# Optimization experiments

Measured on AMD Instinct MI355X. Metric: run time of the kernel, lower is better.

## Reference

```python
import jax, jax.numpy as jnp
import numpy as np

B, S, D, H = 4, 2048, 1024, 16
HD = D // H
EPS = 1e-5

def _ln(x, g, b):
    mu = jnp.mean(x, axis=-1, keepdims=True)
    var = jnp.mean(jnp.square(x - mu), axis=-1, keepdims=True)
    return (x - mu) * jax.lax.rsqrt(var + EPS) * g + b

def setup_inputs() -> dict:
    key = jax.random.key(0)
    ks = jax.random.split(key, 6)
    W = 0.02  # GPT-2 style init scale keeps softmax unsaturated
    causal = jnp.tril(jnp.ones((S, S), dtype=bool))
    mask = jnp.where(causal, 0.0, -1e9).astype(jnp.float32)[None, None]
    return {
        "x": jax.random.normal(ks[0], (B, S, D), jnp.float32),
        "attention_mask": mask,
        "ln1_g": jnp.ones((D,), jnp.float32),
        "ln1_b": jnp.zeros((D,), jnp.float32),
        "w_qkv": jax.random.normal(ks[1], (D, 3 * D), jnp.float32) * W,
        "b_qkv": jnp.zeros((3 * D,), jnp.float32),
        "w_ao": jax.random.normal(ks[2], (D, D), jnp.float32) * W,
        "b_ao": jnp.zeros((D,), jnp.float32),
        "ln2_g": jnp.ones((D,), jnp.float32),
        "ln2_b": jnp.zeros((D,), jnp.float32),
        "w_fc": jax.random.normal(ks[3], (D, 4 * D), jnp.float32) * W,
        "b_fc": jnp.zeros((4 * D,), jnp.float32),
        "w_out": jax.random.normal(ks[4], (4 * D, D), jnp.float32) * W,
        "b_out": jnp.zeros((D,), jnp.float32),
    }

def reference(x, attention_mask, ln1_g, ln1_b, w_qkv, b_qkv, w_ao, b_ao,
              ln2_g, ln2_b, w_fc, b_fc, w_out, b_out):
    b, s, d = x.shape
    h = _ln(x, ln1_g, ln1_b)
    qkv = h @ w_qkv + b_qkv  # [B,S,3D]
    q, k, v = jnp.split(qkv, 3, axis=-1)
    def heads(t):  # [B,S,D] -> [B,H,S,HD]
        return t.reshape(b, s, H, HD).transpose(0, 2, 1, 3)
    q, k, v = heads(q), heads(k), heads(v)
    att = jnp.einsum('bhqd,bhkd->bhqk', q, k) / jnp.sqrt(jnp.float32(HD))
    att = att + attention_mask
    att = jax.nn.softmax(att, axis=-1)
    out = jnp.einsum('bhqk,bhkd->bhqd', att, v)
    out = out.transpose(0, 2, 1, 3).reshape(b, s, d)
    x = x + out @ w_ao + b_ao
    h2 = _ln(x, ln2_g, ln2_b)
    # torch nn.GELU() default is exact erf gelu
    mlp = jax.nn.gelu(h2 @ w_fc + b_fc, approximate=False) @ w_out + b_out
    return x + mlp
```

## Files before the change

kernel.cpp:

```cpp
#include <hip/hip_runtime.h>

typedef unsigned short u16;
typedef __attribute__((ext_vector_type(8))) short short8;
typedef __attribute__((ext_vector_type(4))) float floatx4;

#define S_LEN 2048
#define DMODEL 1024
#define NHEAD 16
#define HDIM 64

__device__ __forceinline__ u16 f2bf(float f) {
    union { float f; unsigned u; } v; v.f = f;
    unsigned u = v.u;
    unsigned r = (u + 0x7fffu + ((u >> 16) & 1u)) >> 16;
    return (u16)r;
}

__device__ __forceinline__ u16 f2bf_fast(float f) {
    union { float f; unsigned u; } v; v.f = f;
    return (u16)((v.u + 0x8000u) >> 16);
}

__device__ __forceinline__ void gld_lds16(const u16* g, u16* l) {
    __builtin_amdgcn_global_load_lds((const __attribute__((address_space(1))) void*)g,
                                     (__attribute__((address_space(3))) void*)l,
                                     16, 0, 0);
}

__global__ __launch_bounds__(256) void ln_kernel(
    const float* __restrict__ x, const float* __restrict__ g,
    const float* __restrict__ b, u16* __restrict__ out)
{
    int row = blockIdx.x;
    int tid = threadIdx.x;
    const float4* xr = (const float4*)(x + (size_t)row * DMODEL);
    float4 v = xr[tid];
    float s  = v.x + v.y + v.z + v.w;
    float s2 = v.x * v.x + v.y * v.y + v.z * v.z + v.w * v.w;
    #pragma unroll
    for (int off = 1; off < 64; off <<= 1) {
        s  += __shfl_xor(s, off, 64);
        s2 += __shfl_xor(s2, off, 64);
    }
    __shared__ float red[2][4];
    int w = tid >> 6, lane = tid & 63;
    if (lane == 0) { red[0][w] = s; red[1][w] = s2; }
    __syncthreads();
    s  = red[0][0] + red[0][1] + red[0][2] + red[0][3];
    s2 = red[1][0] + red[1][1] + red[1][2] + red[1][3];
    float mu  = s * (1.0f / DMODEL);
    float var = s2 * (1.0f / DMODEL) - mu * mu;
    float inv = rsqrtf(var + 1e-5f);
    const float4* gr = (const float4*)g;
    const float4* br = (const float4*)b;
    float4 gv = gr[tid], bv = br[tid];
    u16* o = out + (size_t)row * DMODEL + tid * 4;
    o[0] = f2bf((v.x - mu) * inv * gv.x + bv.x);
    o[1] = f2bf((v.y - mu) * inv * gv.y + bv.y);
    o[2] = f2bf((v.z - mu) * inv * gv.z + bv.z);
    o[3] = f2bf((v.w - mu) * inv * gv.w + bv.w);
}

__global__ __launch_bounds__(256) void transpose_cast(
    const float* __restrict__ w, u16* __restrict__ wt, int K, int N)
{
    __shared__ float t[32][33];
    int n0 = blockIdx.x * 32, k0 = blockIdx.y * 32;
    int x = threadIdx.x, y = threadIdx.y;
    #pragma unroll
    for (int j = y; j < 32; j += 8)
        t[j][x] = w[(size_t)(k0 + j) * N + n0 + x];
    __syncthreads();
    #pragma unroll
    for (int j = y; j < 32; j += 8)
        wt[(size_t)(n0 + j) * K + k0 + x] = f2bf(t[x][j]);
}

__global__ __launch_bounds__(256) void transpose_v(
    const u16* __restrict__ V, u16* __restrict__ Vt)
{
    __shared__ u16 t[64][66];
    int bh = blockIdx.y;
    int s0 = blockIdx.x * 64;
    int lane = threadIdx.x & 63, y = threadIdx.x >> 6;
    const u16* src = V + ((size_t)bh * S_LEN + s0) * HDIM;
    #pragma unroll
    for (int i = 0; i < 16; ++i) {
        int ss = y * 16 + i;
        t[ss][lane] = src[(size_t)ss * HDIM + lane];
    }
    __syncthreads();
    u16* dst = Vt + (size_t)bh * HDIM * S_LEN + s0;
    #pragma unroll
    for (int i = 0; i < 16; ++i) {
        int hd = y * 16 + i;
        dst[(size_t)hd * S_LEN + lane] = t[lane][hd];
    }
}

template<int MODE>
__global__ __launch_bounds__(256) void gemm_bt(
    const u16* __restrict__ A, const u16* __restrict__ BT,
    int M, int N, int K,
    const float* __restrict__ bias, const float* __restrict__ res,
    float* __restrict__ fout,
    u16* __restrict__ o0, u16* __restrict__ o1, u16* __restrict__ o2)
{
    __shared__ __attribute__((aligned(16))) u16 As[128 * 64];
    __shared__ __attribute__((aligned(16))) u16 Bs[128 * 64];
    int tid = threadIdx.x;
    int lane = tid & 63, w = tid >> 6;
    int wm = (w >> 1) * 64, wn = (w & 1) * 64;
    int l15 = lane & 15, quad = lane >> 4;
    int rowBase = blockIdx.y * 128, colBase = blockIdx.x * 128;

    floatx4 acc[4][4] = {};

    for (int k0 = 0; k0 < K; k0 += 64) {
        #pragma unroll
        for (int i = 0; i < 4; ++i) {
            int c  = i * 256 + tid;
            int cb = i * 256 + (tid & 0xC0);
            int r = c >> 3;
            int cs = (c & 7) ^ (r & 7);
            gld_lds16(A  + (size_t)(rowBase + r) * K + k0 + cs * 8, As + (size_t)cb * 8);
            gld_lds16(BT + (size_t)(colBase + r) * K + k0 + cs * 8, Bs + (size_t)cb * 8);
        }
        __syncthreads();
        #pragma unroll
        for (int ks = 0; ks < 2; ++ks) {
            int sw = (((ks * 4 + quad) ^ (l15 & 7))) * 8;
            short8 af[4], bf[4];
            #pragma unroll
            for (int im = 0; im < 4; ++im)
                af[im] = *(const short8*)(As + (wm + im * 16 + l15) * 64 + sw);
            #pragma unroll
            for (int in = 0; in < 4; ++in)
                bf[in] = *(const short8*)(Bs + (wn + in * 16 + l15) * 64 + sw);
            #pragma unroll
            for (int im = 0; im < 4; ++im)
                #pragma unroll
                for (int in = 0; in < 4; ++in)
                    acc[im][in] = __builtin_amdgcn_mfma_f32_16x16x32_bf16(af[im], bf[in], acc[im][in], 0, 0, 0);
        }
        __syncthreads();
    }

    if (MODE == 0) {
        int t = colBase >> 10;
        u16* qb = o0 + (size_t)t * 8388608;
        int cb1023 = colBase & 1023;
        #pragma unroll
        for (int im = 0; im < 4; ++im) {
            #pragma unroll
            for (int in = 0; in < 4; ++in) {
                #pragma unroll
                for (int r = 0; r < 4; ++r) {
                    int gr = rowBase + wm + im * 16 + quad * 4 + r;
                    int gc = colBase + wn + in * 16 + l15;
                    float v = acc[im][in][r] + bias[gc];
                    int rr = cb1023 + wn + in * 16 + l15;
                    int h = rr >> 6, hd = rr & 63;
                    int bb = gr >> 11, ss = gr & 2047;
                    qb[(((size_t)(bb * NHEAD + h) * S_LEN + ss) * HDIM) + hd] = f2bf_fast(v);
                }
            }
        }
    } else {
        #pragma unroll
        for (int im = 0; im < 4; ++im) {
            #pragma unroll
            for (int in = 0; in < 4; ++in) {
                #pragma unroll
                for (int r = 0; r < 4; ++r) {
                    int gr = rowBase + wm + im * 16 + quad * 4 + r;
                    int gc = colBase + wn + in * 16 + l15;
                    float v = acc[im][in][r] + bias[gc];
                    if (MODE == 2) {
                        float p = v * (1.59576912f + 0.07135481f * v * v);
                        float e = __expf(-p);
                        float gl = v * __builtin_amdgcn_rcpf(1.0f + e);
                        o0[(size_t)gr * N + gc] = f2bf_fast(gl);
                    } else {
                        fout[(size_t)gr * N + gc] = v + res[(size_t)gr * N + gc];
                    }
                }
            }
        }
    }
}

__global__ __launch_bounds__(256) void flash_attn(
    const u16* __restrict__ Q, const u16* __restrict__ Kb,
    const u16* __restrict__ Vt, u16* __restrict__ O)
{
    __shared__ __attribute__((aligned(16))) u16 Ks[64 * 64];
    __shared__ __attribute__((aligned(16))) u16 Vs[2][64 * 64];
    __shared__ __attribute__((aligned(16))) u16 Pl[4][16][72];
    int tid = threadIdx.x;
    int lane = tid & 63, w = tid >> 6;
    int l15 = lane & 15, quad = lane >> 4;
    int pr = blockIdx.x;
    int bh = blockIdx.y;
    int bb = bh >> 4, h = bh & 15;

    const u16* Kp0 = Kb + (size_t)bh * S_LEN * HDIM;
    const u16* Vp  = Vt + (size_t)bh * HDIM * S_LEN;

    int rstage = lane >> 3;
    int cstage = ((lane & 7) ^ rstage) * 8;

    #pragma unroll 1
    for (int sel = 0; sel < 2; ++sel) {
        int qt = sel ? (31 - pr) : pr;
        int q0 = qt * 64;

        const u16* Qp = Q + ((size_t)bh * S_LEN + q0 + w * 16) * HDIM;
        short8 aq[2];
        #pragma unroll
        for (int ks = 0; ks < 2; ++ks)
            aq[ks] = *(const short8*)(Qp + l15 * HDIM + ks * 32 + quad * 8);

        floatx4 acc_o[4] = {};
        float rsum[4] = {0.f, 0.f, 0.f, 0.f};

        #pragma unroll 1
        for (int kt = 0; kt <= qt; ++kt) {
            u16* vbuf = (u16*)Vs[kt & 1];
            const u16* Kg = Kp0 + (size_t)kt * 64 * HDIM;
            #pragma unroll
            for (int i = 0; i < 2; ++i) {
                int row = i * 32 + w * 8 + rstage;
                gld_lds16(Kg + row * HDIM + cstage, Ks + i * 2048 + w * 512);
                gld_lds16(Vp + (size_t)row * S_LEN + kt * 64 + cstage, vbuf + i * 2048 + w * 512);
            }
            __syncthreads();

            floatx4 acc_s[4] = {};
            #pragma unroll
            for (int nt = 0; nt < 4; ++nt) {
                #pragma unroll
                for (int ks = 0; ks < 2; ++ks) {
                    int sw = ((ks * 4 + quad) ^ (l15 & 7)) * 8;
                    short8 bk = *(const short8*)(Ks + (nt * 16 + l15) * 64 + sw);
                    acc_s[nt] = __builtin_amdgcn_mfma_f32_16x16x32_bf16(aq[ks], bk, acc_s[nt], 0, 0, 0);
                }
            }
            bool diag = (kt == qt);
            #pragma unroll
            for (int nt = 0; nt < 4; ++nt) {
                #pragma unroll
                for (int r = 0; r < 4; ++r) {
                    float s = acc_s[nt][r] * 0.125f;
                    if (diag) {
                        int kc = nt * 16 + l15;
                        int qr = w * 16 + quad * 4 + r;
                        if (kc > qr) s = -1e30f;
                    }
                    float p = __expf(s);
                    rsum[r] += p;
                    Pl[w][quad * 4 + r][nt * 16 + l15] = f2bf_fast(p);
                }
            }
            __syncthreads();

            short8 pf[2];
            #pragma unroll
            for (int ks = 0; ks < 2; ++ks)
                pf[ks] = *(const short8*)(&Pl[w][l15][ks * 32 + quad * 8]);
            #pragma unroll
            for (int nt = 0; nt < 4; ++nt) {
                #pragma unroll
                for (int ks = 0; ks < 2; ++ks) {
                    int sw = ((ks * 4 + quad) ^ (l15 & 7)) * 8;
                    short8 bv = *(const short8*)(vbuf + (nt * 16 + l15) * 64 + sw);
                    acc_o[nt] = __builtin_amdgcn_mfma_f32_16x16x32_bf16(pf[ks], bv, acc_o[nt], 0, 0, 0);
                }
            }
        }

        float inv[4];
        #pragma unroll
        for (int r = 0; r < 4; ++r) {
            float sm = rsum[r];
            #pragma unroll
            for (int off = 1; off < 16; off <<= 1)
                sm += __shfl_xor(sm, off, 64);
            inv[r] = 1.0f / sm;
        }

        #pragma unroll
        for (int nt = 0; nt < 4; ++nt) {
            #pragma unroll
            for (int r = 0; r < 4; ++r) {
                int qr = q0 + w * 16 + quad * 4 + r;
                int hd = nt * 16 + l15;
                float ov = acc_o[nt][r] * inv[r];
                O[((size_t)bb * S_LEN + qr) * DMODEL + h * HDIM + hd] = f2bf(ov);
            }
        }
        __syncthreads();
    }
}

extern "C" void kernel_launch(void* const* d_in, const int* in_sizes, int n_in,
                              void* d_out, int out_size, void* d_ws, size_t ws_size,
                              hipStream_t stream)
{
    const float* x    = (const float*)d_in[0];
    const float* ln1g = (const float*)d_in[2];
    const float* ln1b = (const float*)d_in[3];
    const float* wqkv = (const float*)d_in[4];
    const float* bqkv = (const float*)d_in[5];
    const float* wao  = (const float*)d_in[6];
    const float* bao  = (const float*)d_in[7];
    const float* ln2g = (const float*)d_in[8];
    const float* ln2b = (const float*)d_in[9];
    const float* wfc  = (const float*)d_in[10];
    const float* bfc  = (const float*)d_in[11];
    const float* wout = (const float*)d_in[12];
    const float* bout = (const float*)d_in[13];
    float* out = (float*)d_out;

    char* ws = (char*)d_ws;
    u16* wqkvT = (u16*)(ws + 0);
    u16* waoT  = (u16*)(ws + 6291456);
    u16* wfcT  = (u16*)(ws + 8388608);
    u16* woutT = (u16*)(ws + 16777216);
    u16* hb    = (u16*)(ws + 25165824);
    u16* QKVb  = (u16*)(ws + 41943040);
    u16* Vtb   = (u16*)(ws + 92274688);
    u16* Gb    = (u16*)(ws + 41943040);

    u16* Qb   = QKVb;
    u16* Kbuf = QKVb + 8388608;
    u16* Vb   = QKVb + 16777216;

    transpose_cast<<<dim3(3072/32, 1024/32), dim3(32, 8), 0, stream>>>(wqkv, wqkvT, 1024, 3072);
    transpose_cast<<<dim3(1024/32, 1024/32), dim3(32, 8), 0, stream>>>(wao,  waoT,  1024, 1024);
    transpose_cast<<<dim3(4096/32, 1024/32), dim3(32, 8), 0, stream>>>(wfc,  wfcT,  1024, 4096);
    transpose_cast<<<dim3(1024/32, 4096/32), dim3(32, 8), 0, stream>>>(wout, woutT, 4096, 1024);

    ln_kernel<<<8192, 256, 0, stream>>>(x, ln1g, ln1b, hb);

    gemm_bt<0><<<dim3(3072/128, 8192/128), 256, 0, stream>>>(
        hb, wqkvT, 8192, 3072, 1024, bqkv, nullptr, nullptr, QKVb, nullptr, nullptr);

    transpose_v<<<dim3(32, 64), 256, 0, stream>>>(Vb, Vtb);

    flash_attn<<<dim3(16, 64), 256, 0, stream>>>(Qb, Kbuf, Vtb, hb);

    gemm_bt<1><<<dim3(1024/128, 8192/128), 256, 0, stream>>>(
        hb, waoT, 8192, 1024, 1024, bao, x, out, nullptr, nullptr, nullptr);

    ln_kernel<<<8192, 256, 0, stream>>>(out, ln2g, ln2b, hb);

    gemm_bt<2><<<dim3(4096/128, 8192/128), 256, 0, stream>>>(
        hb, wfcT, 8192, 4096, 1024, bfc, nullptr, nullptr, Gb, nullptr, nullptr);

    gemm_bt<3><<<dim3(1024/128, 8192/128), 256, 0, stream>>>(
        Gb, woutT, 8192, 1024, 4096, bout, out, out, nullptr, nullptr, nullptr);
}
```

Before: 521.7 us.

## Double-buffer LDS tiles in the bf16 GEMM to overlap loads with MFMA

Splits the GEMM's A and B shared-memory tiles into two buffers. The next K-tile's global-to-LDS loads are issued right after the barrier, so they run while MFMA works on the current tile. This also drops the second barrier per iteration and hoists the per-thread load address math out of the loop. In exchange, LDS use per block doubles to 64KB, which can lower how many blocks fit on each CU.

```diff
diff --git a/kernel.cpp b/kernel.cpp
--- a/kernel.cpp
+++ b/kernel.cpp
@@ -106,8 +106,8 @@
     float* __restrict__ fout,
     u16* __restrict__ o0, u16* __restrict__ o1, u16* __restrict__ o2)
 {
-    __shared__ __attribute__((aligned(16))) u16 As[128 * 64];
-    __shared__ __attribute__((aligned(16))) u16 Bs[128 * 64];
+    __shared__ __attribute__((aligned(16))) u16 As[2][128 * 64];
+    __shared__ __attribute__((aligned(16))) u16 Bs[2][128 * 64];
     int tid = threadIdx.x;
     int lane = tid & 63, w = tid >> 6;
     int wm = (w >> 1) * 64, wn = (w & 1) * 64;
@@ -116,34 +116,55 @@
 
     floatx4 acc[4][4] = {};
 
-    for (int k0 = 0; k0 < K; k0 += 64) {
-        #pragma unroll
-        for (int i = 0; i < 4; ++i) {
-            int c  = i * 256 + tid;
-            int cb = i * 256 + (tid & 0xC0);
-            int r = c >> 3;
-            int cs = (c & 7) ^ (r & 7);
-            gld_lds16(A  + (size_t)(rowBase + r) * K + k0 + cs * 8, As + (size_t)cb * 8);
-            gld_lds16(BT + (size_t)(colBase + r) * K + k0 + cs * 8, Bs + (size_t)cb * 8);
-        }
+    int sr[4], sc[4], scb[4];
+    #pragma unroll
+    for (int i = 0; i < 4; ++i) {
+        int c  = i * 256 + tid;
+        sr[i]  = c >> 3;
+        sc[i]  = ((c & 7) ^ ((c >> 3) & 7)) * 8;
+        scb[i] = (i * 256 + (tid & 0xC0)) * 8;
+    }
+
+    int KT = K >> 6;
+
+    #pragma unroll
+    for (int i = 0; i < 4; ++i) {
+        gld_lds16(A  + (size_t)(rowBase + sr[i]) * K + sc[i], &As[0][0] + scb[i]);
+        gld_lds16(BT + (size_t)(colBase + sr[i]) * K + sc[i], &Bs[0][0] + scb[i]);
+    }
+
+    for (int kt = 0; kt < KT; ++kt) {
         __syncthreads();
+
+        if (kt + 1 < KT) {
+            int k1 = (kt + 1) << 6;
+            u16* abuf = &As[(kt + 1) & 1][0];
+            u16* bbuf = &Bs[(kt + 1) & 1][0];
+            #pragma unroll
+            for (int i = 0; i < 4; ++i) {
+                gld_lds16(A  + (size_t)(rowBase + sr[i]) * K + k1 + sc[i], abuf + scb[i]);
+                gld_lds16(BT + (size_t)(colBase + sr[i]) * K + k1 + sc[i], bbuf + scb[i]);
+            }
+        }
+
+        const u16* as = &As[kt & 1][0];
+        const u16* bs = &Bs[kt & 1][0];
         #pragma unroll
         for (int ks = 0; ks < 2; ++ks) {
             int sw = (((ks * 4 + quad) ^ (l15 & 7))) * 8;
             short8 af[4], bf[4];
             #pragma unroll
             for (int im = 0; im < 4; ++im)
-                af[im] = *(const short8*)(As + (wm + im * 16 + l15) * 64 + sw);
+                af[im] = *(const short8*)(as + (wm + im * 16 + l15) * 64 + sw);
             #pragma unroll
             for (int in = 0; in < 4; ++in)
-                bf[in] = *(const short8*)(Bs + (wn + in * 16 + l15) * 64 + sw);
+                bf[in] = *(const short8*)(bs + (wn + in * 16 + l15) * 64 + sw);
             #pragma unroll
             for (int im = 0; im < 4; ++im)
                 #pragma unroll
                 for (int in = 0; in < 4; ++in)
                     acc[im][in] = __builtin_amdgcn_mfma_f32_16x16x32_bf16(af[im], bf[in], acc[im][in], 0, 0, 0);
         }
-        __syncthreads();
     }
 
     if (MODE == 0) {
```

Measured after the change: 524.1 us. Within noise of the previous version (+0.5%).
